# Performance work log

Measured on AMD Instinct MI355X. Metric: run time of the kernel, lower is better.

Reference implementation:

```python
import jax, jax.numpy as jnp
import numpy as np

N_NODES = 100000
N_EDGES = 3200000
NUM_FEATURES = 128
DIM = 10
NUM_GRAPHS = 64


def setup_inputs() -> dict:
    key = jax.random.key(0)
    k1, k2, k3, k4, k5, k6, k7 = jax.random.split(key, 7)
    features = jax.random.normal(k1, (N_NODES, NUM_FEATURES), dtype=jnp.float32)
    src = jax.random.randint(k2, (N_EDGES,), 0, N_NODES, dtype=jnp.int64)
    dst = jax.random.randint(k3, (N_EDGES,), 0, N_NODES, dtype=jnp.int64)
    graph_ids = jnp.sort(jax.random.randint(k4, (N_NODES,), 0, NUM_GRAPHS, dtype=jnp.int64))
    # GraphConv weights (no bias), glorot-ish scaling
    W1 = jax.random.normal(k5, (NUM_FEATURES, DIM), dtype=jnp.float32) / np.sqrt(NUM_FEATURES)
    W2 = jax.random.normal(k6, (DIM, DIM), dtype=jnp.float32) / np.sqrt(DIM)
    W3 = jax.random.normal(k7, (DIM, 1), dtype=jnp.float32) / np.sqrt(DIM)
    return {"features": features, "W1": W1, "W2": W2, "W3": W3,
            "src": src, "dst": dst, "graph_ids": graph_ids}


def _sum_aggregate(h, src, dst, n_nodes):
    # message = h[src], reduce-sum at dst (norm='none' GraphConv aggregation)
    return jax.ops.segment_sum(h[src], dst, num_segments=n_nodes)


def reference(features, W1, W2, W3, src, dst, graph_ids):
    n = features.shape[0]
    # conv1: in_feats(128) > out_feats(10) -> weight first, then aggregate
    h = features @ W1                          # [N, DIM]
    h = _sum_aggregate(h, src, dst, n)         # [N, DIM]
    h = jax.nn.relu(h)
    # conv2: in_feats == out_feats -> aggregate first, then weight
    h = _sum_aggregate(h, src, dst, n) @ W2    # [N, DIM]
    # dgl.mean_nodes: per-graph mean pooling over nodes
    sums = jax.ops.segment_sum(h, graph_ids, num_segments=NUM_GRAPHS)           # [G, DIM]
    cnt = jax.ops.segment_sum(jnp.ones((n, 1), h.dtype), graph_ids, num_segments=NUM_GRAPHS)
    pooled = sums / jnp.maximum(cnt, 1.0)      # [G, DIM]
    return jax.nn.sigmoid(pooled @ W3)         # [G, 1]
```

## Files before the change

kernel.cpp:

```cpp
#include <hip/hip_runtime.h>
#include <hip/hip_fp16.h>

#define N_NODES 100000
#define N_EDGES 3200000
#define NUM_FEATURES 128
#define DIM 10
#define NUM_GRAPHS 64

#define BSHIFT 8
#define BSIZE (1 << BSHIFT)
#define NB ((N_NODES + BSIZE - 1) / BSIZE)
#define CHUNKS 2
#define PCHUNKS 4
#define EPB 12500
#define PLACE_BLOCKS 256
#define GEMM_BLOCKS 6250
#define BOUND_BLOCKS 196
#define TILE (BSIZE * DIM)
#define CAP 4608
#define CAPB 16384
#define NCHUNK (NB * CHUNKS)
#define NCHUNK2 (NB * PCHUNKS)
#define ACC_STRIDE 11

__global__ __launch_bounds__(512) void k_front(const float* __restrict__ feat,
                                               const float* __restrict__ W1,
                                               __half* __restrict__ h1,
                                               const int* __restrict__ gids,
                                               int* __restrict__ bound,
                                               const int* __restrict__ src,
                                               const int* __restrict__ dst,
                                               int* __restrict__ cnt,
                                               int* __restrict__ pk) {
    __shared__ int hd[NB];
    __shared__ int cb[NB];

    if (blockIdx.x < PLACE_BLOCKS) {
        int base0 = blockIdx.x * EPB;
        for (int t = threadIdx.x; t < NB; t += 512) hd[t] = 0;
        __syncthreads();

        {
            int i = threadIdx.x;
            for (; i + 1536 < EPB; i += 2048) {
                int d0 = dst[base0 + i],        d1 = dst[base0 + i + 512];
                int d2 = dst[base0 + i + 1024], d3 = dst[base0 + i + 1536];
                atomicAdd(&hd[d0 >> BSHIFT], 1);
                atomicAdd(&hd[d1 >> BSHIFT], 1);
                atomicAdd(&hd[d2 >> BSHIFT], 1);
                atomicAdd(&hd[d3 >> BSHIFT], 1);
            }
            for (; i < EPB; i += 512) {
                int d = dst[base0 + i];
                atomicAdd(&hd[d >> BSHIFT], 1);
            }
        }
        __syncthreads();

        for (int t = threadIdx.x; t < NB; t += 512) {
            int c = hd[t];
            int o = c ? atomicAdd(&cnt[t], c) : 0;
            cb[t] = t * CAPB + o;
        }
        __syncthreads();

        {
            int i = threadIdx.x;
            for (; i + 1536 < EPB; i += 2048) {
                int d0 = dst[base0 + i],        d1 = dst[base0 + i + 512];
                int d2 = dst[base0 + i + 1024], d3 = dst[base0 + i + 1536];
                int s0 = src[base0 + i],        s1 = src[base0 + i + 512];
                int s2 = src[base0 + i + 1024], s3 = src[base0 + i + 1536];
                int q0 = atomicAdd(&cb[d0 >> BSHIFT], 1);
                int q1 = atomicAdd(&cb[d1 >> BSHIFT], 1);
                int q2 = atomicAdd(&cb[d2 >> BSHIFT], 1);
                int q3 = atomicAdd(&cb[d3 >> BSHIFT], 1);
                if (q0 < ((d0 >> BSHIFT) + 1) * CAPB) pk[q0] = ((d0 & (BSIZE - 1)) << 17) | s0;
                if (q1 < ((d1 >> BSHIFT) + 1) * CAPB) pk[q1] = ((d1 & (BSIZE - 1)) << 17) | s1;
                if (q2 < ((d2 >> BSHIFT) + 1) * CAPB) pk[q2] = ((d2 & (BSIZE - 1)) << 17) | s2;
                if (q3 < ((d3 >> BSHIFT) + 1) * CAPB) pk[q3] = ((d3 & (BSIZE - 1)) << 17) | s3;
            }
            for (; i < EPB; i += 512) {
                int d = dst[base0 + i];
                int s = src[base0 + i];
                int q = atomicAdd(&cb[d >> BSHIFT], 1);
                if (q < ((d >> BSHIFT) + 1) * CAPB) pk[q] = ((d & (BSIZE - 1)) << 17) | s;
            }
        }
        return;
    }

    int bb = blockIdx.x - PLACE_BLOCKS;

    int nb2 = bb * 512 + threadIdx.x;
    if (bb < BOUND_BLOCKS && nb2 < N_NODES) {
        int g  = gids[nb2];
        int gp = nb2 ? gids[nb2 - 1] : -1;
        for (int v = gp + 1; v <= g; ++v) bound[v] = nb2;
        if (nb2 == N_NODES - 1)
            for (int v = g + 1; v <= NUM_GRAPHS; ++v) bound[v] = N_NODES;
    }

    int gid  = bb * 512 + threadIdx.x;
    int node = gid >> 5;
    int lane = gid & 31;
    if (node >= N_NODES) return;

    float w[4][DIM];
#pragma unroll
    for (int j = 0; j < 4; ++j)
#pragma unroll
        for (int k = 0; k < DIM; ++k)
            w[j][k] = W1[(lane * 4 + j) * DIM + k];

    const float4 f = *reinterpret_cast<const float4*>(feat + (size_t)node * NUM_FEATURES + lane * 4);
    float fv[4] = {f.x, f.y, f.z, f.w};

    float acc[DIM];
#pragma unroll
    for (int k = 0; k < DIM; ++k) acc[k] = 0.f;
#pragma unroll
    for (int j = 0; j < 4; ++j)
#pragma unroll
        for (int k = 0; k < DIM; ++k)
            acc[k] += fv[j] * w[j][k];

#pragma unroll
    for (int off = 16; off > 0; off >>= 1)
#pragma unroll
        for (int k = 0; k < DIM; ++k)
            acc[k] += __shfl_xor(acc[k], off);

    if (lane == 0) {
        __half2* o = (__half2*)h1;
#pragma unroll
        for (int j = 0; j < 5; ++j)
            o[(size_t)node * 5 + j] = __floats2half2_rn(acc[2 * j], acc[2 * j + 1]);
    }
}

__global__ __launch_bounds__(512) void k_spmm1(const __half* __restrict__ h,
                                               const int* __restrict__ cnt,
                                               const int* __restrict__ pk,
                                               float* __restrict__ part) {
    __shared__ int eh[CAP];
    __shared__ int srt[CAP];
    __shared__ int hist[BSIZE];
    __shared__ int cur[BSIZE];

    int b     = blockIdx.x / CHUNKS;
    int chunk = blockIdx.x % CHUNKS;
    int s0  = b * CAPB;
    int len = cnt[b];
    int c0  = s0 + (len * chunk) / CHUNKS;
    int c1  = s0 + (len * (chunk + 1)) / CHUNKS;
    int n   = c1 - c0;
    int nc  = min(n, CAP);

    for (int t = threadIdx.x; t < BSIZE; t += 512) hist[t] = 0;
    __syncthreads();

    {
        int i = threadIdx.x;
        for (; i + 1536 < nc; i += 2048) {
            int p0 = pk[c0 + i],        p1 = pk[c0 + i + 512];
            int p2 = pk[c0 + i + 1024], p3 = pk[c0 + i + 1536];
            eh[i] = p0; eh[i + 512] = p1; eh[i + 1024] = p2; eh[i + 1536] = p3;
            atomicAdd(&hist[p0 >> 17], 1);
            atomicAdd(&hist[p1 >> 17], 1);
            atomicAdd(&hist[p2 >> 17], 1);
            atomicAdd(&hist[p3 >> 17], 1);
        }
        for (; i < nc; i += 512) {
            int p = pk[c0 + i];
            eh[i] = p;
            atomicAdd(&hist[p >> 17], 1);
        }
    }
    __syncthreads();

    if (threadIdx.x < 64) {
        int l = threadIdx.x;
        int carry = 0;
#pragma unroll
        for (int j = 0; j < 4; ++j) {
            int x = hist[j * 64 + l];
            int v = x;
#pragma unroll
            for (int off = 1; off < 64; off <<= 1) {
                int t2 = __shfl_up(v, off);
                if (l >= off) v += t2;
            }
            cur[j * 64 + l] = carry + v - x;
            carry += __shfl(v, 63);
        }
    }
    __syncthreads();

    for (int i = threadIdx.x; i < nc; i += 512) {
        int p = eh[i];
        int pos = atomicAdd(&cur[p >> 17], 1);
        srt[pos] = p;
    }
    __syncthreads();

    int wave = threadIdx.x >> 6;
    int lane = threadIdx.x & 63;
    int slot = lane / 5;
    int l    = lane - slot * 5;
    float* pb = part + (size_t)blockIdx.x * TILE;
    const __half2* h2 = (const __half2*)h;

    if (slot < 12) {
        int g = wave * 12 + slot;
        for (int loc = g; loc < BSIZE; loc += 96) {
            int e0 = loc ? cur[loc - 1] : 0;
            int e1 = cur[loc];
            float ax0 = 0.f, ay0 = 0.f, ax1 = 0.f, ay1 = 0.f;
            float ax2 = 0.f, ay2 = 0.f, ax3 = 0.f, ay3 = 0.f;
            int e = e0;
            for (; e + 7 < e1; e += 8) {
                float2 v0 = __half22float2(h2[(size_t)(srt[e]     & 0x1FFFF) * 5 + l]);
                float2 v1 = __half22float2(h2[(size_t)(srt[e + 1] & 0x1FFFF) * 5 + l]);
                float2 v2 = __half22float2(h2[(size_t)(srt[e + 2] & 0x1FFFF) * 5 + l]);
                float2 v3 = __half22float2(h2[(size_t)(srt[e + 3] & 0x1FFFF) * 5 + l]);
                float2 v4 = __half22float2(h2[(size_t)(srt[e + 4] & 0x1FFFF) * 5 + l]);
                float2 v5 = __half22float2(h2[(size_t)(srt[e + 5] & 0x1FFFF) * 5 + l]);
                float2 v6 = __half22float2(h2[(size_t)(srt[e + 6] & 0x1FFFF) * 5 + l]);
                float2 v7 = __half22float2(h2[(size_t)(srt[e + 7] & 0x1FFFF) * 5 + l]);
                ax0 += v0.x + v4.x; ay0 += v0.y + v4.y;
                ax1 += v1.x + v5.x; ay1 += v1.y + v5.y;
                ax2 += v2.x + v6.x; ay2 += v2.y + v6.y;
                ax3 += v3.x + v7.x; ay3 += v3.y + v7.y;
            }
            for (; e < e1; ++e) {
                float2 v = __half22float2(h2[(size_t)(srt[e] & 0x1FFFF) * 5 + l]);
                ax0 += v.x; ay0 += v.y;
            }
            pb[loc * DIM + 2 * l]     = (ax0 + ax1) + (ax2 + ax3);
            pb[loc * DIM + 2 * l + 1] = (ay0 + ay1) + (ay2 + ay3);
        }
    }
    __syncthreads();

    for (int i = CAP + threadIdx.x; i < n; i += 512) {
        int p = pk[c0 + i];
        int loc = p >> 17, s = p & 0x1FFFF;
#pragma unroll
        for (int j = 0; j < 5; ++j) {
            float2 v = __half22float2(h2[(size_t)s * 5 + j]);
            atomicAdd(&pb[loc * DIM + 2 * j], v.x);
            atomicAdd(&pb[loc * DIM + 2 * j + 1], v.y);
        }
    }
}

__global__ __launch_bounds__(256) void k_merge_relu(const float* __restrict__ part,
                                                    __half* __restrict__ r) {
    int b     = blockIdx.x;
    int nbase = b << BSHIFT;
    const float* p0 = part + (size_t)(b * CHUNKS) * TILE;
    __half2* r2 = (__half2*)r;
    for (int t = threadIdx.x; t < TILE / 2; t += 256) {
        float sx = 0.f, sy = 0.f;
#pragma unroll
        for (int c = 0; c < CHUNKS; ++c) {
            float2 v = ((const float2*)(p0 + (size_t)c * TILE))[t];
            sx += v.x; sy += v.y;
        }
        int ebase = nbase * DIM + 2 * t;
        if (ebase < N_NODES * DIM)
            r2[(size_t)nbase * 5 + t] = __floats2half2_rn(fmaxf(sx, 0.f), fmaxf(sy, 0.f));
    }
}

__global__ __launch_bounds__(512) void k_pass2(const __half* __restrict__ r,
                                               const int* __restrict__ cnt,
                                               const int* __restrict__ pk,
                                               const int* __restrict__ bound,
                                               float* __restrict__ sums) {
    __shared__ float acc[NUM_GRAPHS * ACC_STRIDE];

    int b     = blockIdx.x / PCHUNKS;
    int chunk = blockIdx.x % PCHUNKS;
    int nbase = b << BSHIFT;
    int nlast = min(nbase + BSIZE - 1, N_NODES - 1);

    int glo = 0, ghx = NUM_GRAPHS - 1;
#pragma unroll
    for (int it = 0; it < 6; ++it) {
        int mid = (glo + ghx + 1) >> 1;
        if (bound[mid] <= nbase) glo = mid; else ghx = mid - 1;
    }
    int lo2 = 0, hi2 = NUM_GRAPHS - 1;
#pragma unroll
    for (int it = 0; it < 6; ++it) {
        int mid = (lo2 + hi2 + 1) >> 1;
        if (bound[mid] <= nlast) lo2 = mid; else hi2 = mid - 1;
    }
    int ghi  = lo2;
    int span = ghi - glo;

    for (int t = threadIdx.x; t < (span + 1) * DIM; t += 512)
        acc[(glo + t / DIM) * ACC_STRIDE + t % DIM] = 0.f;
    __syncthreads();

    int s0  = b * CAPB;
    int len = cnt[b];
    int c0  = s0 + (len * chunk) / PCHUNKS;
    int c1  = s0 + (len * (chunk + 1)) / PCHUNKS;

    int wave = threadIdx.x >> 6;
    int lane = threadIdx.x & 63;
    int slot = lane / 5;
    int l    = lane - slot * 5;
    const __half2* r2 = (const __half2*)r;

    if (slot < 12) {
        const int STR = 96;
        int q = wave * 12 + slot;
        int e = c0 + q;
        if (span <= 1) {
            int gA  = glo;
            int gB  = (span == 1) ? glo + 1 : glo;
            int cut = (span == 1) ? (bound[glo + 1] - nbase) : BSIZE;
            float axA = 0.f, ayA = 0.f, axB = 0.f, ayB = 0.f;
            for (; e + 7 * STR < c1; e += 8 * STR) {
                int p[8];
#pragma unroll
                for (int u = 0; u < 8; ++u) p[u] = pk[e + u * STR];
                float2 v[8];
#pragma unroll
                for (int u = 0; u < 8; ++u)
                    v[u] = __half22float2(r2[(size_t)(p[u] & 0x1FFFF) * 5 + l]);
#pragma unroll
                for (int u = 0; u < 8; ++u) {
                    bool a = (p[u] >> 17) < cut;
                    axA += a ? v[u].x : 0.f;  ayA += a ? v[u].y : 0.f;
                    axB += a ? 0.f : v[u].x;  ayB += a ? 0.f : v[u].y;
                }
            }
            for (; e < c1; e += STR) {
                int p = pk[e];
                float2 v = __half22float2(r2[(size_t)(p & 0x1FFFF) * 5 + l]);
                bool a = (p >> 17) < cut;
                axA += a ? v.x : 0.f;  ayA += a ? v.y : 0.f;
                axB += a ? 0.f : v.x;  ayB += a ? 0.f : v.y;
            }
            atomicAdd(&acc[gA * ACC_STRIDE + 2 * l], axA);
            atomicAdd(&acc[gA * ACC_STRIDE + 2 * l + 1], ayA);
            if (span == 1) {
                atomicAdd(&acc[gB * ACC_STRIDE + 2 * l], axB);
                atomicAdd(&acc[gB * ACC_STRIDE + 2 * l + 1], ayB);
            }
        } else {
            for (; e < c1; e += STR) {
                int p   = pk[e];
                int loc = p >> 17;
                float2 v = __half22float2(r2[(size_t)(p & 0x1FFFF) * 5 + l]);
                int g = glo;
                for (int gg = glo + 1; gg <= ghi; ++gg)
                    g += (loc >= bound[gg] - nbase) ? 1 : 0;
                atomicAdd(&acc[g * ACC_STRIDE + 2 * l], v.x);
                atomicAdd(&acc[g * ACC_STRIDE + 2 * l + 1], v.y);
            }
        }
    }
    __syncthreads();

    for (int t = threadIdx.x; t < (span + 1) * DIM; t += 512) {
        int g = glo + t / DIM;
        float v = acc[g * ACC_STRIDE + t % DIM];
        if (v != 0.f) atomicAdd(&sums[g * DIM + t % DIM], v);
    }
}

__global__ void k_final(const float* __restrict__ sums, const int* __restrict__ bound,
                        const float* __restrict__ W2, const float* __restrict__ W3,
                        float* __restrict__ out) {
    int g = threadIdx.x;
    if (g >= NUM_GRAPHS) return;
    float c = fmaxf((float)(bound[g + 1] - bound[g]), 1.f);
    float p[DIM];
#pragma unroll
    for (int k = 0; k < DIM; ++k) p[k] = sums[g * DIM + k] / c;
    float z = 0.f;
#pragma unroll
    for (int j = 0; j < DIM; ++j) {
        float t = 0.f;
#pragma unroll
        for (int k = 0; k < DIM; ++k) t += p[k] * W2[k * DIM + j];
        z += t * W3[j];
    }
    out[g] = 1.f / (1.f + expf(-z));
}

extern "C" void kernel_launch(void* const* d_in, const int* in_sizes, int n_in,
                              void* d_out, int out_size, void* d_ws, size_t ws_size,
                              hipStream_t stream) {
    const float* feat = (const float*)d_in[0];
    const float* W1   = (const float*)d_in[1];
    const float* W2   = (const float*)d_in[2];
    const float* W3   = (const float*)d_in[3];
    const int*   src  = (const int*)d_in[4];
    const int*   dst  = (const int*)d_in[5];
    const int*   gids = (const int*)d_in[6];
    float*       out  = (float*)d_out;

    char* ws = (char*)d_ws;
    __half* h1    = (__half*)(ws);
    int*    pk    = (int*)(ws + 2000000);
    __half* r     = (__half*)(ws + 27624576);
    float*  part  = (float*)(ws + 29624576);
    int*    cnt   = (int*)(ws + 37632256);
    float*  sums  = (float*)(ws + 37633824);
    int*    bound = (int*)(ws + 37636384);

    hipMemsetAsync(ws + 37632256, 0, 4128, stream);

    k_front<<<PLACE_BLOCKS + GEMM_BLOCKS, 512, 0, stream>>>(feat, W1, h1, gids, bound,
                                                            src, dst, cnt, pk);
    k_spmm1     <<<NCHUNK, 512, 0, stream>>>(h1, cnt, pk, part);
    k_merge_relu<<<NB, 256, 0, stream>>>(part, r);
    k_pass2     <<<NCHUNK2, 512, 0, stream>>>(r, cnt, pk, bound, sums);

    k_final<<<1, 64, 0, stream>>>(sums, bound, W2, W3, out);
}
```

Measured before the change: 215.5 us.

## Compute W1 projection with one thread per output element using shared W1

The dense feature-by-W1 projection no longer uses a 32-lane warp per node with shuffle reductions. Each thread now computes one output element as a full 128-long dot product, with W1 transposed into padded shared memory, which cuts the block count from 6250 to 1954. This removes the shuffle-reduction traffic and the redundant per-lane weight loads. In exchange, each of the 10 threads for a node rereads that node's 512-byte feature row (relying on cache), and the tail blocks of the placement path now reserve extra shared memory.

Measured after the change: 223.8 us. 3.8% more time.

```diff
diff --git a/kernel.cpp b/kernel.cpp
--- a/kernel.cpp
+++ b/kernel.cpp
@@ -14,7 +14,8 @@
 #define PCHUNKS 4
 #define EPB 12500
 #define PLACE_BLOCKS 256
-#define GEMM_BLOCKS 6250
+#define NOUT (N_NODES * DIM)
+#define GEMM_BLOCKS 1954
 #define BOUND_BLOCKS 196
 #define TILE (BSIZE * DIM)
 #define CAP 4608
@@ -22,6 +23,7 @@
 #define NCHUNK (NB * CHUNKS)
 #define NCHUNK2 (NB * PCHUNKS)
 #define ACC_STRIDE 11
+#define W1T_LD 132
 
 __global__ __launch_bounds__(512) void k_front(const float* __restrict__ feat,
                                                const float* __restrict__ W1,
@@ -34,6 +36,7 @@
                                                int* __restrict__ pk) {
     __shared__ int hd[NB];
     __shared__ int cb[NB];
+    __shared__ float w1t[DIM * W1T_LD];
 
     if (blockIdx.x < PLACE_BLOCKS) {
         int base0 = blockIdx.x * EPB;
@@ -50,10 +53,8 @@
                 atomicAdd(&hd[d2 >> BSHIFT], 1);
                 atomicAdd(&hd[d3 >> BSHIFT], 1);
             }
-            for (; i < EPB; i += 512) {
-                int d = dst[base0 + i];
-                atomicAdd(&hd[d >> BSHIFT], 1);
-            }
+            for (; i < EPB; i += 512)
+                atomicAdd(&hd[dst[base0 + i] >> BSHIFT], 1);
         }
         __syncthreads();
 
@@ -101,42 +102,32 @@
             for (int v = g + 1; v <= NUM_GRAPHS; ++v) bound[v] = N_NODES;
     }
 
-    int gid  = bb * 512 + threadIdx.x;
-    int node = gid >> 5;
-    int lane = gid & 31;
-    if (node >= N_NODES) return;
-
-    float w[4][DIM];
-#pragma unroll
-    for (int j = 0; j < 4; ++j)
-#pragma unroll
-        for (int k = 0; k < DIM; ++k)
-            w[j][k] = W1[(lane * 4 + j) * DIM + k];
-
-    const float4 f = *reinterpret_cast<const float4*>(feat + (size_t)node * NUM_FEATURES + lane * 4);
-    float fv[4] = {f.x, f.y, f.z, f.w};
-
-    float acc[DIM];
-#pragma unroll
-    for (int k = 0; k < DIM; ++k) acc[k] = 0.f;
-#pragma unroll
-    for (int j = 0; j < 4; ++j)
-#pragma unroll
-        for (int k = 0; k < DIM; ++k)
-            acc[k] += fv[j] * w[j][k];
-
-#pragma unroll
-    for (int off = 16; off > 0; off >>= 1)
-#pragma unroll
-        for (int k = 0; k < DIM; ++k)
-            acc[k] += __shfl_xor(acc[k], off);
-
-    if (lane == 0) {
-        __half2* o = (__half2*)h1;
-#pragma unroll
-        for (int j = 0; j < 5; ++j)
-            o[(size_t)node * 5 + j] = __floats2half2_rn(acc[2 * j], acc[2 * j + 1]);
-    }
+    for (int idx = threadIdx.x; idx < NUM_FEATURES * DIM; idx += 512) {
+        int j = idx / DIM;
+        int k = idx - j * DIM;
+        w1t[k * W1T_LD + j] = W1[idx];
+    }
+    __syncthreads();
+
+    int ot = bb * 512 + threadIdx.x;
+    if (ot >= NOUT) return;
+    int n = ot / DIM;
+    int k = ot - n * DIM;
+
+    const float4* f4 = reinterpret_cast<const float4*>(feat) + (size_t)n * (NUM_FEATURES / 4);
+    const float* wk = &w1t[k * W1T_LD];
+
+    float a0 = 0.f, a1 = 0.f, a2 = 0.f, a3 = 0.f;
+#pragma unroll
+    for (int m = 0; m < NUM_FEATURES / 4; ++m) {
+        float4 fv = f4[m];
+        float4 wv = *reinterpret_cast<const float4*>(wk + 4 * m);
+        a0 += fv.x * wv.x;
+        a1 += fv.y * wv.y;
+        a2 += fv.z * wv.z;
+        a3 += fv.w * wv.w;
+    }
+    h1[ot] = __float2half_rn((a0 + a1) + (a2 + a3));
 }
 
 __global__ __launch_bounds__(512) void k_spmm1(const __half* __restrict__ h,
```
